# Optimization experiments

Hardware: AMD Instinct MI355X
Metric: run time of the kernel (lower is better)

Reference implementation:

```python
import jax, jax.numpy as jnp
import numpy as np


def setup_inputs() -> dict:
    key = jax.random.key(0)
    k1, k2 = jax.random.split(key)
    N, C = 16384, 1000
    feature = jax.random.normal(k1, (N, C), dtype=jnp.float32)
    label = jax.random.randint(k2, (N,), 0, C, dtype=jnp.int64)
    return {"feature": feature, "label": label}


def reference(feature, label):
    # feature: [N, C] logits, label: [N] int class ids
    N, C = feature.shape
    log_p = jax.nn.log_softmax(feature, axis=1)          # stable log(softmax)
    p = jnp.exp(log_p)                                   # soft_output
    beta = (1.0 - p) ** 2                                # focal-style modulation

    # ni = number of samples in the batch sharing this sample's label
    # (replaces the O(N*C) python loops with bincount + gather)
    counts = jnp.zeros((C,), dtype=feature.dtype).at[label].add(1.0)
    ni = counts[label]                                   # [N]
    r = ni / N                                           # class frequency ratio
    alpha = jnp.exp(r - 1.0) / r                         # cost-sensitive weight, [N]

    cs_feature = alpha[:, None] * beta * log_p           # [N, C]
    # NLLLoss (mean reduction): -mean(cs_feature[i, label[i]])
    picked = jnp.take_along_axis(cs_feature, label[:, None], axis=1)[:, 0]
    return -jnp.mean(picked)
```

## Files before the change

### kernel.cpp

```cpp
#include <hip/hip_runtime.h>
#include <math.h>

#define N_ROWS 16384
#define N_COLS 1000
#define WAVES_PER_BLOCK 4
#define MAIN_BLOCKS (N_ROWS / WAVES_PER_BLOCK)

__global__ __launch_bounds__(1024) void bincount_kernel(
    const int* __restrict__ label, float* __restrict__ counts) {
  __shared__ int cnt[N_COLS];
  for (int i = threadIdx.x; i < N_COLS; i += 1024) cnt[i] = 0;
  __syncthreads();
  for (int j = threadIdx.x; j < N_ROWS; j += 1024) {
    atomicAdd(&cnt[label[j]], 1);
  }
  __syncthreads();
  for (int i = threadIdx.x; i < N_COLS; i += 1024) counts[i] = (float)cnt[i];
}

__global__ __launch_bounds__(256) void rowloss_kernel(
    const float* __restrict__ feature, const int* __restrict__ label,
    const float* __restrict__ counts, float* __restrict__ partial) {
  const int wave = threadIdx.x >> 6;
  const int lane = threadIdx.x & 63;
  const int row  = blockIdx.x * WAVES_PER_BLOCK + wave;

  const float* rowp = feature + (size_t)row * N_COLS;

  float4 v[4];
#pragma unroll
  for (int k = 0; k < 4; ++k) {
    const int e = k * 256 + lane * 4;
    if (e < N_COLS) {
      v[k] = *reinterpret_cast<const float4*>(rowp + e);
    } else {
      v[k] = make_float4(-INFINITY, -INFINITY, -INFINITY, -INFINITY);
    }
  }

  float m = -INFINITY;
#pragma unroll
  for (int k = 0; k < 4; ++k) {
    m = fmaxf(m, fmaxf(fmaxf(v[k].x, v[k].y), fmaxf(v[k].z, v[k].w)));
  }
#pragma unroll
  for (int off = 32; off > 0; off >>= 1) m = fmaxf(m, __shfl_xor(m, off));

  const float LOG2E = 1.4426950408889634f;
  const float mL = m * LOG2E;
  float s = 0.0f;
#pragma unroll
  for (int k = 0; k < 4; ++k) {
    s += exp2f(fmaf(v[k].x, LOG2E, -mL));
    s += exp2f(fmaf(v[k].y, LOG2E, -mL));
    s += exp2f(fmaf(v[k].z, LOG2E, -mL));
    s += exp2f(fmaf(v[k].w, LOG2E, -mL));
  }
#pragma unroll
  for (int off = 32; off > 0; off >>= 1) s += __shfl_xor(s, off);

  __shared__ float wsum[WAVES_PER_BLOCK];
  if (lane == 0) {
    const int lab = label[row];
    const float xl = rowp[lab];
    const float logp = xl - m - logf(s);
    const float p = expf(logp);
    float b = 1.0f - p;
    b = b * b;
    const float ni = counts[lab];
    const float r = ni * (1.0f / (float)N_ROWS);
    const float alpha = expf(r - 1.0f) / r;
    wsum[wave] = alpha * b * logp;
  }
  __syncthreads();
  if (threadIdx.x == 0) {
    partial[blockIdx.x] = wsum[0] + wsum[1] + wsum[2] + wsum[3];
  }
}

__global__ __launch_bounds__(1024) void reduce_kernel(
    const float* __restrict__ partial, float* __restrict__ out) {
  __shared__ float lds[1024];
  float s = 0.0f;
  for (int i = threadIdx.x; i < MAIN_BLOCKS; i += 1024) s += partial[i];
  lds[threadIdx.x] = s;
  __syncthreads();
  for (int off = 512; off > 0; off >>= 1) {
    if (threadIdx.x < off) lds[threadIdx.x] += lds[threadIdx.x + off];
    __syncthreads();
  }
  if (threadIdx.x == 0) out[0] = -lds[0] * (1.0f / (float)N_ROWS);
}

extern "C" void kernel_launch(void* const* d_in, const int* in_sizes, int n_in,
                              void* d_out, int out_size, void* d_ws, size_t ws_size,
                              hipStream_t stream) {
  const float* feature = (const float*)d_in[0];
  const int*   label   = (const int*)d_in[1];
  float* counts  = (float*)d_ws;
  float* partial = (float*)d_ws + 1024;
  float* out     = (float*)d_out;

  bincount_kernel<<<1, 1024, 0, stream>>>(label, counts);
  rowloss_kernel<<<MAIN_BLOCKS, 256, 0, stream>>>(feature, label, counts, partial);
  reduce_kernel<<<1, 1024, 0, stream>>>(partial, out);
}
```

Measured before the change: 97.33 us.

## Fuse final reduction into row kernel via atomics and enlarge blocks

Removes the separate reduce kernel: each row-loss block now reduces its wave results and atomically adds the scaled sum into the output, which the bincount kernel zeroes. Blocks grow from 4 to 16 waves, the bincount loop is vectorized with int4 label loads, and the label, count and picked-logit loads are hoisted so they overlap with the row load. This saves one kernel launch and the partial-buffer round trip. In exchange it adds float atomics on a single address, which makes the summation order nondeterministic.

```diff
diff --git a/kernel.cpp b/kernel.cpp
--- a/kernel.cpp
+++ b/kernel.cpp
@@ -3,29 +3,45 @@
 
 #define N_ROWS 16384
 #define N_COLS 1000
-#define WAVES_PER_BLOCK 4
+#define WAVES_PER_BLOCK 16
 #define MAIN_BLOCKS (N_ROWS / WAVES_PER_BLOCK)
 
 __global__ __launch_bounds__(1024) void bincount_kernel(
-    const int* __restrict__ label, float* __restrict__ counts) {
+    const int* __restrict__ label, int* __restrict__ counts,
+    float* __restrict__ out) {
   __shared__ int cnt[N_COLS];
   for (int i = threadIdx.x; i < N_COLS; i += 1024) cnt[i] = 0;
+  if (threadIdx.x == 0) out[0] = 0.0f;
   __syncthreads();
-  for (int j = threadIdx.x; j < N_ROWS; j += 1024) {
-    atomicAdd(&cnt[label[j]], 1);
-  }
+
+  const int4* __restrict__ l4 = reinterpret_cast<const int4*>(label);
+  int4 a = l4[threadIdx.x];
+  int4 b = l4[threadIdx.x + 1024];
+  int4 c = l4[threadIdx.x + 2048];
+  int4 d = l4[threadIdx.x + 3072];
+  atomicAdd(&cnt[a.x], 1); atomicAdd(&cnt[a.y], 1);
+  atomicAdd(&cnt[a.z], 1); atomicAdd(&cnt[a.w], 1);
+  atomicAdd(&cnt[b.x], 1); atomicAdd(&cnt[b.y], 1);
+  atomicAdd(&cnt[b.z], 1); atomicAdd(&cnt[b.w], 1);
+  atomicAdd(&cnt[c.x], 1); atomicAdd(&cnt[c.y], 1);
+  atomicAdd(&cnt[c.z], 1); atomicAdd(&cnt[c.w], 1);
+  atomicAdd(&cnt[d.x], 1); atomicAdd(&cnt[d.y], 1);
+  atomicAdd(&cnt[d.z], 1); atomicAdd(&cnt[d.w], 1);
   __syncthreads();
-  for (int i = threadIdx.x; i < N_COLS; i += 1024) counts[i] = (float)cnt[i];
+  for (int i = threadIdx.x; i < N_COLS; i += 1024) counts[i] = cnt[i];
 }
 
-__global__ __launch_bounds__(256) void rowloss_kernel(
+__global__ __launch_bounds__(1024) void rowloss_kernel(
     const float* __restrict__ feature, const int* __restrict__ label,
-    const float* __restrict__ counts, float* __restrict__ partial) {
+    const int* __restrict__ counts, float* __restrict__ out) {
   const int wave = threadIdx.x >> 6;
   const int lane = threadIdx.x & 63;
   const int row  = blockIdx.x * WAVES_PER_BLOCK + wave;
+  const float* rowp = feature + (size_t)row * N_COLS;
 
-  const float* rowp = feature + (size_t)row * N_COLS;
+  const int   lab = label[row];
+  const float ni  = (float)counts[lab];
+  const float xl  = rowp[lab];
 
   float4 v[4];
 #pragma unroll
@@ -38,11 +54,10 @@
     }
   }
 
-  float m = -INFINITY;
+  float m = fmaxf(fmaxf(v[0].x, v[0].y), fmaxf(v[0].z, v[0].w));
 #pragma unroll
-  for (int k = 0; k < 4; ++k) {
+  for (int k = 1; k < 4; ++k)
     m = fmaxf(m, fmaxf(fmaxf(v[k].x, v[k].y), fmaxf(v[k].z, v[k].w)));
-  }
 #pragma unroll
   for (int off = 32; off > 0; off >>= 1) m = fmaxf(m, __shfl_xor(m, off));
 
@@ -59,37 +74,25 @@
 #pragma unroll
   for (int off = 32; off > 0; off >>= 1) s += __shfl_xor(s, off);
 
+  const float logp  = xl - m - logf(s);
+  const float p     = expf(logp);
+  const float beta  = (1.0f - p) * (1.0f - p);
+  const float r     = ni * (1.0f / (float)N_ROWS);
+  const float alpha = expf(r - 1.0f) / r;
+  const float val   = alpha * beta * logp;
+
   __shared__ float wsum[WAVES_PER_BLOCK];
-  if (lane == 0) {
-    const int lab = label[row];
-    const float xl = rowp[lab];
-    const float logp = xl - m - logf(s);
-    const float p = expf(logp);
-    float b = 1.0f - p;
-    b = b * b;
-    const float ni = counts[lab];
-    const float r = ni * (1.0f / (float)N_ROWS);
-    const float alpha = expf(r - 1.0f) / r;
-    wsum[wave] = alpha * b * logp;
+  if (lane == 0) wsum[wave] = val;
+  __syncthreads();
+
+  if (threadIdx.x < WAVES_PER_BLOCK) {
+    float t = wsum[threadIdx.x];
+#pragma unroll
+    for (int off = WAVES_PER_BLOCK / 2; off > 0; off >>= 1)
+      t += __shfl_xor(t, off);
+    if (threadIdx.x == 0)
+      atomicAdd(out, t * (-1.0f / (float)N_ROWS));
   }
-  __syncthreads();
-  if (threadIdx.x == 0) {
-    partial[blockIdx.x] = wsum[0] + wsum[1] + wsum[2] + wsum[3];
-  }
-}
-
-__global__ __launch_bounds__(1024) void reduce_kernel(
-    const float* __restrict__ partial, float* __restrict__ out) {
-  __shared__ float lds[1024];
-  float s = 0.0f;
-  for (int i = threadIdx.x; i < MAIN_BLOCKS; i += 1024) s += partial[i];
-  lds[threadIdx.x] = s;
-  __syncthreads();
-  for (int off = 512; off > 0; off >>= 1) {
-    if (threadIdx.x < off) lds[threadIdx.x] += lds[threadIdx.x + off];
-    __syncthreads();
-  }
-  if (threadIdx.x == 0) out[0] = -lds[0] * (1.0f / (float)N_ROWS);
 }
 
 extern "C" void kernel_launch(void* const* d_in, const int* in_sizes, int n_in,
@@ -97,11 +100,9 @@
                               hipStream_t stream) {
   const float* feature = (const float*)d_in[0];
   const int*   label   = (const int*)d_in[1];
-  float* counts  = (float*)d_ws;
-  float* partial = (float*)d_ws + 1024;
-  float* out     = (float*)d_out;
+  int*   counts = (int*)d_ws;
+  float* out    = (float*)d_out;
 
-  bincount_kernel<<<1, 1024, 0, stream>>>(label, counts);
-  rowloss_kernel<<<MAIN_BLOCKS, 256, 0, stream>>>(feature, label, counts, partial);
-  reduce_kernel<<<1, 1024, 0, stream>>>(partial, out);
+  bincount_kernel<<<1, 1024, 0, stream>>>(label, counts, out);
+  rowloss_kernel<<<MAIN_BLOCKS, 1024, 0, stream>>>(feature, label, counts, out);
 }
```

Result: slower. 99.43 us (+2.2%).

## Fold bincount into row kernel via per-class atomics, apply alpha in finalize

Applied to the files above, without the earlier changes.

Removes the single-block serial bincount kernel. Since alpha depends only on the class, the row kernel now atomically accumulates beta*logp and a count per class, and a finalize kernel applies alpha per class and reduces. A memset replaces the first kernel. This trades a serial 16K-label histogram launch for global atomics spread over 1000 addresses, which may contend.

```diff
diff --git a/kernel.cpp b/kernel.cpp
--- a/kernel.cpp
+++ b/kernel.cpp
@@ -6,43 +6,30 @@
 #define WAVES_PER_BLOCK 4
 #define MAIN_BLOCKS (N_ROWS / WAVES_PER_BLOCK)
 
-__global__ __launch_bounds__(1024) void bincount_kernel(
-    const int* __restrict__ label, float* __restrict__ counts) {
-  __shared__ int cnt[N_COLS];
-  for (int i = threadIdx.x; i < N_COLS; i += 1024) cnt[i] = 0;
-  __syncthreads();
-  for (int j = threadIdx.x; j < N_ROWS; j += 1024) {
-    atomicAdd(&cnt[label[j]], 1);
-  }
-  __syncthreads();
-  for (int i = threadIdx.x; i < N_COLS; i += 1024) counts[i] = (float)cnt[i];
-}
 
 __global__ __launch_bounds__(256) void rowloss_kernel(
     const float* __restrict__ feature, const int* __restrict__ label,
-    const float* __restrict__ counts, float* __restrict__ partial) {
+    float* __restrict__ S, int* __restrict__ cnt) {
   const int wave = threadIdx.x >> 6;
   const int lane = threadIdx.x & 63;
   const int row  = blockIdx.x * WAVES_PER_BLOCK + wave;
+  const float* rowp = feature + (size_t)row * N_COLS;
 
-  const float* rowp = feature + (size_t)row * N_COLS;
+  const int   lab = label[row];
+  const float xl  = rowp[lab];
 
   float4 v[4];
 #pragma unroll
   for (int k = 0; k < 4; ++k) {
     const int e = k * 256 + lane * 4;
-    if (e < N_COLS) {
-      v[k] = *reinterpret_cast<const float4*>(rowp + e);
-    } else {
-      v[k] = make_float4(-INFINITY, -INFINITY, -INFINITY, -INFINITY);
-    }
+    v[k] = (e < N_COLS) ? *reinterpret_cast<const float4*>(rowp + e)
+                        : make_float4(-INFINITY, -INFINITY, -INFINITY, -INFINITY);
   }
 
-  float m = -INFINITY;
+  float m = fmaxf(fmaxf(v[0].x, v[0].y), fmaxf(v[0].z, v[0].w));
 #pragma unroll
-  for (int k = 0; k < 4; ++k) {
+  for (int k = 1; k < 4; ++k)
     m = fmaxf(m, fmaxf(fmaxf(v[k].x, v[k].y), fmaxf(v[k].z, v[k].w)));
-  }
 #pragma unroll
   for (int off = 32; off > 0; off >>= 1) m = fmaxf(m, __shfl_xor(m, off));
 
@@ -59,31 +46,29 @@
 #pragma unroll
   for (int off = 32; off > 0; off >>= 1) s += __shfl_xor(s, off);
 
-  __shared__ float wsum[WAVES_PER_BLOCK];
-  if (lane == 0) {
-    const int lab = label[row];
-    const float xl = rowp[lab];
-    const float logp = xl - m - logf(s);
-    const float p = expf(logp);
-    float b = 1.0f - p;
-    b = b * b;
-    const float ni = counts[lab];
-    const float r = ni * (1.0f / (float)N_ROWS);
-    const float alpha = expf(r - 1.0f) / r;
-    wsum[wave] = alpha * b * logp;
-  }
-  __syncthreads();
-  if (threadIdx.x == 0) {
-    partial[blockIdx.x] = wsum[0] + wsum[1] + wsum[2] + wsum[3];
-  }
+  const float logp = xl - m - logf(s);
+  const float p    = expf(logp);
+  const float beta = (1.0f - p) * (1.0f - p);
+
+  if (lane == 0) atomicAdd(&S[lab], beta * logp);
+  if (lane == 1) atomicAdd(&cnt[lab], 1);
 }
 
-__global__ __launch_bounds__(1024) void reduce_kernel(
-    const float* __restrict__ partial, float* __restrict__ out) {
+__global__ __launch_bounds__(1024) void finalize_kernel(
+    const float* __restrict__ S, const int* __restrict__ cnt,
+    float* __restrict__ out) {
   __shared__ float lds[1024];
-  float s = 0.0f;
-  for (int i = threadIdx.x; i < MAIN_BLOCKS; i += 1024) s += partial[i];
-  lds[threadIdx.x] = s;
+  float t = 0.0f;
+  const int c = threadIdx.x;
+  if (c < N_COLS) {
+    const int n = cnt[c];
+    if (n > 0) {
+      const float r = (float)n * (1.0f / (float)N_ROWS);
+      const float alpha = expf(r - 1.0f) / r;
+      t = alpha * S[c];
+    }
+  }
+  lds[threadIdx.x] = t;
   __syncthreads();
   for (int off = 512; off > 0; off >>= 1) {
     if (threadIdx.x < off) lds[threadIdx.x] += lds[threadIdx.x + off];
@@ -97,11 +82,11 @@
                               hipStream_t stream) {
   const float* feature = (const float*)d_in[0];
   const int*   label   = (const int*)d_in[1];
-  float* counts  = (float*)d_ws;
-  float* partial = (float*)d_ws + 1024;
-  float* out     = (float*)d_out;
+  float* S   = (float*)d_ws;
+  int*   cnt = (int*)d_ws + 1024;
+  float* out = (float*)d_out;
 
-  bincount_kernel<<<1, 1024, 0, stream>>>(label, counts);
-  rowloss_kernel<<<MAIN_BLOCKS, 256, 0, stream>>>(feature, label, counts, partial);
-  reduce_kernel<<<1, 1024, 0, stream>>>(partial, out);
+  hipMemsetAsync(d_ws, 0, 8192, stream);
+  rowloss_kernel<<<MAIN_BLOCKS, 256, 0, stream>>>(feature, label, S, cnt);
+  finalize_kernel<<<1, 1024, 0, stream>>>(S, cnt, out);
 }
```

Measured after the change: 94.42 us. -3.0%, faster.
